# Kernel optimization log

Hardware: AMD Instinct MI355X
Metric: run time of the kernel (lower is better)

Reference implementation:

```python
import jax, jax.numpy as jnp
import numpy as np

D_MODEL = 512
NUM_HEADS = 8
D_K = D_MODEL // NUM_HEADS


def setup_inputs() -> dict:
    key = jax.random.key(0)
    kx, kq, kk, kv, ko = jax.random.split(key, 5)
    scale = 1.0 / np.sqrt(D_MODEL)
    return {
        "x": jax.random.normal(kx, (2, 4096, D_MODEL), dtype=jnp.float32),
        "Wq": jax.random.normal(kq, (D_MODEL, D_MODEL), dtype=jnp.float32) * scale,
        "Wk": jax.random.normal(kk, (D_MODEL, D_MODEL), dtype=jnp.float32) * scale,
        "Wv": jax.random.normal(kv, (D_MODEL, D_MODEL), dtype=jnp.float32) * scale,
        "Wo": jax.random.normal(ko, (D_MODEL, D_MODEL), dtype=jnp.float32) * scale,
    }


def reference(x, Wq, Wk, Wv, Wo):
    B, T, D = x.shape
    H, dk = NUM_HEADS, D_K
    # Linear(d,d, bias=False): y = x @ W.T ; weights stored [out,in] like torch
    q = (x @ Wq.T).reshape(B, T, H, dk).transpose(0, 2, 1, 3)  # [B,H,T,dk]
    k = (x @ Wk.T).reshape(B, T, H, dk).transpose(0, 2, 1, 3)
    v = (x @ Wv.T).reshape(B, T, H, dk).transpose(0, 2, 1, 3)
    scores = jnp.einsum("bhqd,bhkd->bhqk", q, k) / np.sqrt(dk)  # [B,H,T,T]
    probs = jax.nn.softmax(scores, axis=-1)
    o = jnp.einsum("bhqk,bhkd->bhqd", probs, v)  # [B,H,T,dk]
    o = o.transpose(0, 2, 1, 3).reshape(B, T, D)
    return o @ Wo.T
```

## Files before the change

### kernel.cpp

```cpp
#include <hip/hip_runtime.h>
#include <hip/hip_bf16.h>

#define SEQ 4096
#define DMODEL 512
#define HEADS 8
#define DK 64
#define BATCH 2
#define MTOT (BATCH * SEQ)
#define NBH (BATCH * HEADS)

typedef __attribute__((ext_vector_type(8))) short bh8;
typedef __attribute__((ext_vector_type(4))) float f4;
typedef __attribute__((ext_vector_type(16))) float f16x;

#define MFMA(a, b, c)   __builtin_amdgcn_mfma_f32_16x16x32_bf16(a, b, c, 0, 0, 0)
#define MFMA32(a, b, c) __builtin_amdgcn_mfma_f32_32x32x16_bf16(a, b, c, 0, 0, 0)
#define GLL16(g, l) __builtin_amdgcn_global_load_lds( \
    (const __attribute__((address_space(1))) void*)(g), \
    (__attribute__((address_space(3))) void*)(l), 16, 0, 0)

__device__ __forceinline__ unsigned short f2b(float f) {
    union { float f; unsigned u; } v; v.f = f;
    unsigned r = v.u + 0x7fff + ((v.u >> 16) & 1);
    return (unsigned short)(r >> 16);
}

__device__ __forceinline__ unsigned cvtpk(float lo, float hi) {
    unsigned r;
    asm("v_cvt_pk_bf16_f32 %0, %1, %2" : "=v"(r) : "v"(lo), "v"(hi));
    return r;
}
__device__ __forceinline__ void plswap(unsigned& a, unsigned& b) {
    asm("v_permlane32_swap_b32 %0, %1" : "+v"(a), "+v"(b));
}
__device__ __forceinline__ float wave_max_pair(float x) {
    float b = x; asm("" : "+v"(b));
    float a = x;
    asm("v_permlane32_swap_b32 %0, %1" : "+v"(a), "+v"(b));
    return fmaxf(a, b);
}
__device__ __forceinline__ float wave_sum_pair(float x) {
    float b = x; asm("" : "+v"(b));
    float a = x;
    asm("v_permlane32_swap_b32 %0, %1" : "+v"(a), "+v"(b));
    return a + b;
}

__global__ __launch_bounds__(256) void convert_k(
    const float* __restrict__ x, const float* __restrict__ wq,
    const float* __restrict__ wk, const float* __restrict__ wv,
    const float* __restrict__ wo, unsigned short* __restrict__ dst)
{
    const size_t i = ((size_t)blockIdx.x * 256 + threadIdx.x) * 4;
    const float* s; size_t o;
    if (i < 4194304u)                 { s = x;  o = i; }
    else if (i < 4194304u + 262144u)  { s = wq; o = i - 4194304u; }
    else if (i < 4194304u + 524288u)  { s = wk; o = i - (4194304u + 262144u); }
    else if (i < 4194304u + 786432u)  { s = wv; o = i - (4194304u + 524288u); }
    else                              { s = wo; o = i - (4194304u + 786432u); }
    float4 v = *(const float4*)(s + o);
    ushort4 u; u.x = f2b(v.x); u.y = f2b(v.y); u.z = f2b(v.z); u.w = f2b(v.w);
    *(ushort4*)(dst + i) = u;
}

__global__ __launch_bounds__(256) void qkv_gemm_mfma(
    const unsigned short* __restrict__ xb,
    const unsigned short* __restrict__ Wb,
    unsigned short* __restrict__ QKV)
{
    const int z = blockIdx.z;
    const unsigned short* A = xb;
    const unsigned short* B = Wb + (size_t)z * (DMODEL * DMODEL);
    const int m0 = blockIdx.x * 128, n0 = blockIdx.y * 128;
    const int tid = threadIdx.x, w = tid >> 6, l = tid & 63;
    const int wr = w >> 1, wc = w & 1;

    __shared__ __align__(16) unsigned short As[128 * 32];
    __shared__ __align__(16) unsigned short Bs[128 * 32];

    f4 acc[4][4] = {};
    const int lrow = l >> 2, lslot = l & 3;

    for (int k0 = 0; k0 < DMODEL; k0 += 32) {
        __syncthreads();
        #pragma unroll
        for (int j = 0; j < 2; ++j) {
            const int row = w * 32 + j * 16 + lrow;
            const int sw = lslot ^ ((row >> 1) & 3);
            GLL16(A + (size_t)(m0 + row) * DMODEL + k0 + sw * 8,
                  (char*)As + (w * 32 + j * 16) * 64);
            GLL16(B + (size_t)(n0 + row) * DMODEL + k0 + sw * 8,
                  (char*)Bs + (w * 32 + j * 16) * 64);
        }
        __syncthreads();
        bh8 af[4], bg[4];
        #pragma unroll
        for (int mi = 0; mi < 4; ++mi) {
            const int r = wr * 64 + mi * 16 + (l & 15);
            af[mi] = *(const bh8*)((const char*)As + r * 64 +
                                   (((l >> 4) * 16) ^ (((r >> 1) & 3) << 4)));
        }
        #pragma unroll
        for (int ni = 0; ni < 4; ++ni) {
            const int r = wc * 64 + ni * 16 + (l & 15);
            bg[ni] = *(const bh8*)((const char*)Bs + r * 64 +
                                   (((l >> 4) * 16) ^ (((r >> 1) & 3) << 4)));
        }
        #pragma unroll
        for (int mi = 0; mi < 4; ++mi)
            #pragma unroll
            for (int ni = 0; ni < 4; ++ni)
                acc[mi][ni] = MFMA(af[mi], bg[ni], acc[mi][ni]);
    }

    unsigned short* Out = QKV + (size_t)z * ((size_t)NBH * SEQ * DK);
    const float sc = (z == 0) ? 0.18033688011112042f : 1.0f;
    #pragma unroll
    for (int mi = 0; mi < 4; ++mi) {
        #pragma unroll
        for (int rg = 0; rg < 4; ++rg) {
            const int m = m0 + wr * 64 + mi * 16 + (l >> 4) * 4 + rg;
            const int b = m >> 12, t = m & (SEQ - 1);
            #pragma unroll
            for (int ni = 0; ni < 4; ++ni) {
                const int n = n0 + wc * 64 + ni * 16 + (l & 15);
                const int h = n >> 6, d = n & 63;
                Out[(((size_t)(b * HEADS + h)) * SEQ + t) * DK + d] =
                    f2b(acc[mi][ni][rg] * sc);
            }
        }
    }
}

__global__ __launch_bounds__(256) void vtrans(
    const unsigned short* __restrict__ Vh, unsigned short* __restrict__ Vt)
{
    const int bh = blockIdx.y, t0 = blockIdx.x * 64;
    __shared__ unsigned short L[64][72];
    const unsigned short* src = Vh + ((size_t)bh * SEQ + t0) * DK;
    const int r = threadIdx.x >> 3, c8 = (threadIdx.x & 7) * 8;
    #pragma unroll
    for (int it = 0; it < 2; ++it) {
        const int row = r + it * 32;
        ushort4 a = *(const ushort4*)(src + (size_t)row * DK + c8);
        ushort4 b = *(const ushort4*)(src + (size_t)row * DK + c8 + 4);
        L[row][c8 + 0] = a.x; L[row][c8 + 1] = a.y; L[row][c8 + 2] = a.z; L[row][c8 + 3] = a.w;
        L[row][c8 + 4] = b.x; L[row][c8 + 5] = b.y; L[row][c8 + 6] = b.z; L[row][c8 + 7] = b.w;
    }
    __syncthreads();
    unsigned short* dst = Vt + (size_t)bh * DK * SEQ + t0;
    #pragma unroll
    for (int it = 0; it < 2; ++it) {
        const int d = r + it * 32;
        ushort4 a, b;
        a.x = L[c8 + 0][d]; a.y = L[c8 + 1][d]; a.z = L[c8 + 2][d]; a.w = L[c8 + 3][d];
        b.x = L[c8 + 4][d]; b.y = L[c8 + 5][d]; b.z = L[c8 + 6][d]; b.w = L[c8 + 7][d];
        *(ushort4*)(dst + (size_t)d * SEQ + c8) = a;
        *(ushort4*)(dst + (size_t)d * SEQ + c8 + 4) = b;
    }
}

__global__ __launch_bounds__(256) void flash_mfma(
    const unsigned short* __restrict__ Qh,
    const unsigned short* __restrict__ Kh,
    const unsigned short* __restrict__ Vtp,
    unsigned short* __restrict__ Ow)
{
    const int bid = blockIdx.x;
    const int bh = bid & 15, q0 = (bid >> 4) * 128;
    const int tid = threadIdx.x, w = tid >> 6, l = tid & 63;
    const int lq = l & 31, hi = l >> 5;

    __shared__ __align__(16) unsigned short Ks[2][64 * 64];
    __shared__ __align__(16) unsigned short Vs[2][64 * 64];

    const unsigned short* Qb = Qh + (size_t)bh * SEQ * DK;
    const unsigned short* Kb = Kh + (size_t)bh * SEQ * DK;
    const unsigned short* Vb = Vtp + (size_t)bh * DK * SEQ;

    bh8 qf[4];
    #pragma unroll
    for (int ks = 0; ks < 4; ++ks)
        qf[ks] = *(const bh8*)(Qb + (size_t)(q0 + w * 32 + lq) * DK + ks * 16 + hi * 8);

    f16x o0 = {}, o1 = {};
    float m_run = -3.0e38f, l_run = 0.f;

    const int srow = l >> 3, sslot = l & 7;

#define STAGE(buf, kv0_) do {                                                 \
    _Pragma("unroll")                                                         \
    for (int j_ = 0; j_ < 2; ++j_) {                                          \
        const int row_ = w * 16 + j_ * 8 + srow;                              \
        const int sw_ = sslot ^ (row_ & 7);                                   \
        GLL16(Kb + (size_t)((kv0_) + row_) * DK + sw_ * 8,                    \
              (char*)Ks[buf] + (w * 16 + j_ * 8) * 128);                      \
        GLL16(Vb + (size_t)row_ * SEQ + (kv0_) + sw_ * 8,                     \
              (char*)Vs[buf] + (w * 16 + j_ * 8) * 128);                      \
    }                                                                         \
} while (0)

    STAGE(0, 0);
    __syncthreads();
    int cur = 0;

    for (int t = 0; t < SEQ / 64; ++t) {
        if (t < SEQ / 64 - 1) STAGE(cur ^ 1, (t + 1) * 64);

        const char* kb = (const char*)Ks[cur];
        const char* vb = (const char*)Vs[cur];

        f16x sa0 = {}, sa1 = {};
        __builtin_amdgcn_s_setprio(1);
        #pragma unroll
        for (int ks = 0; ks < 4; ++ks) {
            const int boff = ks * 32 + hi * 16;
            const int r0 = lq, r1 = 32 + lq;
            bh8 k0 = *(const bh8*)(kb + r0 * 128 + (boff ^ ((r0 & 7) << 4)));
            bh8 k1 = *(const bh8*)(kb + r1 * 128 + (boff ^ ((r1 & 7) << 4)));
            sa0 = MFMA32(k0, qf[ks], sa0);
            sa1 = MFMA32(k1, qf[ks], sa1);
        }
        __builtin_amdgcn_s_setprio(0);

        float t0 = -3.0e38f, t1 = -3.0e38f, t2 = -3.0e38f, t3 = -3.0e38f;
        #pragma unroll
        for (int r = 0; r < 16; r += 4) {
            t0 = fmaxf(t0, fmaxf(sa0[r + 0], sa1[r + 0]));
            t1 = fmaxf(t1, fmaxf(sa0[r + 1], sa1[r + 1]));
            t2 = fmaxf(t2, fmaxf(sa0[r + 2], sa1[r + 2]));
            t3 = fmaxf(t3, fmaxf(sa0[r + 3], sa1[r + 3]));
        }
        const float mx = wave_max_pair(fmaxf(fmaxf(t0, t1), fmaxf(t2, t3)));

        const bool skip = __all(mx <= m_run + 8.0f);
        float mnew = m_run, corr = 1.0f;
        if (!skip) {
            mnew = fmaxf(m_run, mx);
            corr = __builtin_amdgcn_exp2f(m_run - mnew);
        }

        float p[32];
        #pragma unroll
        for (int r = 0; r < 16; ++r) {
            p[r]      = __builtin_amdgcn_exp2f(sa0[r] - mnew);
            p[16 + r] = __builtin_amdgcn_exp2f(sa1[r] - mnew);
        }
        float a0 = 0.f, a1 = 0.f, a2 = 0.f, a3 = 0.f;
        #pragma unroll
        for (int r = 0; r < 32; r += 4) {
            a0 += p[r + 0]; a1 += p[r + 1]; a2 += p[r + 2]; a3 += p[r + 3];
        }
        const float psum = wave_sum_pair((a0 + a1) + (a2 + a3));

        if (!skip) {
            m_run = mnew;
            l_run = l_run * corr + psum;
            #pragma unroll
            for (int r = 0; r < 16; ++r) { o0[r] *= corr; o1[r] *= corr; }
        } else {
            l_run += psum;
        }

        bh8 pf[4];
        #pragma unroll
        for (int cb = 0; cb < 2; ++cb) {
            const int b0 = cb * 16;
            unsigned k0 = cvtpk(p[b0 + 0],  p[b0 + 1]);
            unsigned k1 = cvtpk(p[b0 + 2],  p[b0 + 3]);
            unsigned k2 = cvtpk(p[b0 + 4],  p[b0 + 5]);
            unsigned k3 = cvtpk(p[b0 + 6],  p[b0 + 7]);
            unsigned k4 = cvtpk(p[b0 + 8],  p[b0 + 9]);
            unsigned k5 = cvtpk(p[b0 + 10], p[b0 + 11]);
            unsigned k6 = cvtpk(p[b0 + 12], p[b0 + 13]);
            unsigned k7 = cvtpk(p[b0 + 14], p[b0 + 15]);
            plswap(k0, k2);
            plswap(k1, k3);
            plswap(k4, k6);
            plswap(k5, k7);
            union { unsigned u[4]; bh8 v; } f0, f1;
            f0.u[0] = k0; f0.u[1] = k1; f0.u[2] = k2; f0.u[3] = k3;
            f1.u[0] = k4; f1.u[1] = k5; f1.u[2] = k6; f1.u[3] = k7;
            pf[cb * 2 + 0] = f0.v;
            pf[cb * 2 + 1] = f1.v;
        }

        __builtin_amdgcn_s_setprio(1);
        #pragma unroll
        for (int ks = 0; ks < 4; ++ks) {
            const int boff = ks * 32 + hi * 16;
            const int r0 = lq, r1 = 32 + lq;
            bh8 v0 = *(const bh8*)(vb + r0 * 128 + (boff ^ ((r0 & 7) << 4)));
            bh8 v1 = *(const bh8*)(vb + r1 * 128 + (boff ^ ((r1 & 7) << 4)));
            o0 = MFMA32(v0, pf[ks], o0);
            o1 = MFMA32(v1, pf[ks], o1);
        }
        __builtin_amdgcn_s_setprio(0);

        __syncthreads();
        cur ^= 1;
    }
#undef STAGE

    const float inv = 1.0f / l_run;
    char* Tb = (char*)Ks + w * 4096;
    #pragma unroll
    for (int db = 0; db < 2; ++db) {
        f16x ov = db ? o1 : o0;
        #pragma unroll
        for (int j = 0; j < 8; ++j) {
            const int r = 2 * j;
            const int d = db * 32 + (r & 3) + 8 * (r >> 2) + 4 * hi;
            unsigned pk = cvtpk(ov[r] * inv, ov[r + 1] * inv);
            *(unsigned*)(Tb + lq * 128 + ((d * 2) ^ ((lq & 7) << 4))) = pk;
        }
    }
    __syncthreads();
    const int b = bh >> 3, h = bh & 7;
    const int row = l >> 1, half = l & 1;
    const int q = q0 + w * 32 + row;
    unsigned short* dst = Ow + ((size_t)b * SEQ + q) * DMODEL + h * DK + half * 32;
    #pragma unroll
    for (int i = 0; i < 4; ++i) {
        const int byte = (half * 64 + i * 16) ^ ((row & 7) << 4);
        uint4 vv = *(const uint4*)(Tb + row * 128 + byte);
        *(uint4*)(dst + i * 8) = vv;
    }
}

__global__ __launch_bounds__(256) void out_gemm_mfma(
    const unsigned short* __restrict__ Ob,
    const unsigned short* __restrict__ Wob,
    float* __restrict__ out)
{
    const int m0 = blockIdx.x * 128, n0 = blockIdx.y * 128;
    const int tid = threadIdx.x, w = tid >> 6, l = tid & 63;
    const int wr = w >> 1, wc = w & 1;

    __shared__ __align__(16) unsigned short As[128 * 32];
    __shared__ __align__(16) unsigned short Bs[128 * 32];

    f4 acc[4][4] = {};
    const int lrow = l >> 2, lslot = l & 3;

    for (int k0 = 0; k0 < DMODEL; k0 += 32) {
        __syncthreads();
        #pragma unroll
        for (int j = 0; j < 2; ++j) {
            const int row = w * 32 + j * 16 + lrow;
            const int sw = lslot ^ ((row >> 1) & 3);
            GLL16(Ob + (size_t)(m0 + row) * DMODEL + k0 + sw * 8,
                  (char*)As + (w * 32 + j * 16) * 64);
            GLL16(Wob + (size_t)(n0 + row) * DMODEL + k0 + sw * 8,
                  (char*)Bs + (w * 32 + j * 16) * 64);
        }
        __syncthreads();
        bh8 af[4], bg[4];
        #pragma unroll
        for (int mi = 0; mi < 4; ++mi) {
            const int r = wr * 64 + mi * 16 + (l & 15);
            af[mi] = *(const bh8*)((const char*)As + r * 64 +
                                   (((l >> 4) * 16) ^ (((r >> 1) & 3) << 4)));
        }
        #pragma unroll
        for (int ni = 0; ni < 4; ++ni) {
            const int r = wc * 64 + ni * 16 + (l & 15);
            bg[ni] = *(const bh8*)((const char*)Bs + r * 64 +
                                   (((l >> 4) * 16) ^ (((r >> 1) & 3) << 4)));
        }
        #pragma unroll
        for (int mi = 0; mi < 4; ++mi)
            #pragma unroll
            for (int ni = 0; ni < 4; ++ni)
                acc[mi][ni] = MFMA(af[mi], bg[ni], acc[mi][ni]);
    }

    #pragma unroll
    for (int mi = 0; mi < 4; ++mi) {
        #pragma unroll
        for (int rg = 0; rg < 4; ++rg) {
            const int m = m0 + wr * 64 + mi * 16 + (l >> 4) * 4 + rg;
            #pragma unroll
            for (int ni = 0; ni < 4; ++ni) {
                const int n = n0 + wc * 64 + ni * 16 + (l & 15);
                out[(size_t)m * DMODEL + n] = acc[mi][ni][rg];
            }
        }
    }
}

extern "C" void kernel_launch(void* const* d_in, const int* in_sizes, int n_in,
                              void* d_out, int out_size, void* d_ws, size_t ws_size,
                              hipStream_t stream)
{
    const float* x  = (const float*)d_in[0];
    const float* Wq = (const float*)d_in[1];
    const float* Wk = (const float*)d_in[2];
    const float* Wv = (const float*)d_in[3];
    const float* Wo = (const float*)d_in[4];
    float* out = (float*)d_out;

    unsigned short* ws = (unsigned short*)d_ws;
    unsigned short* xb  = ws;
    unsigned short* Wb  = xb + 4194304;
    unsigned short* QKV = Wb + 4 * 262144;
    unsigned short* Vt  = QKV + 3 * 4194304;
    unsigned short* Ow  = Vt + 4194304;
    unsigned short* Qh = QKV;
    unsigned short* Kh = QKV + 4194304;
    unsigned short* Vh = QKV + 2 * 4194304;

    convert_k<<<5120, 256, 0, stream>>>(x, Wq, Wk, Wv, Wo, ws);
    qkv_gemm_mfma<<<dim3(MTOT / 128, DMODEL / 128, 3), 256, 0, stream>>>(xb, Wb, QKV);
    vtrans<<<dim3(SEQ / 64, NBH), 256, 0, stream>>>(Vh, Vt);
    flash_mfma<<<512, 256, 0, stream>>>(Qh, Kh, Vt, Ow);
    out_gemm_mfma<<<dim3(MTOT / 128, DMODEL / 128), 256, 0, stream>>>(
        Ow, Wb + 3 * 262144, out);
}
```

Measured before the change: 145.4 us.

## Stage K/V tiles in MFMA-fragment order and pack softmax math

The K and V tiles are now loaded into LDS already arranged as per-lane MFMA fragments, so each lane reads contiguous 16-byte chunks at fixed offsets. This replaces the swizzled row addressing and its XOR math, and the global loads become less contiguous per row. The softmax inner loop also uses v_max3 for the row max and packed f32 add and multiply for the subtract, the sum and the output rescale. These cut VALU instruction count in the loop between the MFMAs.

Measured after the change: 154.0 us. 1.06x slower.

```diff
diff --git a/kernel.cpp b/kernel.cpp
--- a/kernel.cpp
+++ b/kernel.cpp
@@ -12,6 +12,7 @@
 typedef __attribute__((ext_vector_type(8))) short bh8;
 typedef __attribute__((ext_vector_type(4))) float f4;
 typedef __attribute__((ext_vector_type(16))) float f16x;
+typedef __attribute__((ext_vector_type(2))) float f2;
 
 #define MFMA(a, b, c)   __builtin_amdgcn_mfma_f32_16x16x32_bf16(a, b, c, 0, 0, 0)
 #define MFMA32(a, b, c) __builtin_amdgcn_mfma_f32_32x32x16_bf16(a, b, c, 0, 0, 0)
@@ -44,6 +45,16 @@
     float a = x;
     asm("v_permlane32_swap_b32 %0, %1" : "+v"(a), "+v"(b));
     return a + b;
+}
+__device__ __forceinline__ f2 pk_add(f2 a, f2 b) {
+    f2 d; asm("v_pk_add_f32 %0, %1, %2" : "=v"(d) : "v"(a), "v"(b)); return d;
+}
+__device__ __forceinline__ f2 pk_mul(f2 a, f2 b) {
+    f2 d; asm("v_pk_mul_f32 %0, %1, %2" : "=v"(d) : "v"(a), "v"(b)); return d;
+}
+__device__ __forceinline__ float max3f(float a, float b, float c) {
+    float d; asm("v_max3_f32 %0, %1, %2, %3" : "=v"(d) : "v"(a), "v"(b), "v"(c));
+    return d;
 }
 
 __global__ __launch_bounds__(256) void convert_k(
@@ -171,8 +182,7 @@
     const int tid = threadIdx.x, w = tid >> 6, l = tid & 63;
     const int lq = l & 31, hi = l >> 5;
 
-    __shared__ __align__(16) unsigned short Ks[2][64 * 64];
-    __shared__ __align__(16) unsigned short Vs[2][64 * 64];
+    __shared__ __align__(16) char lds[32768];
 
     const unsigned short* Qb = Qh + (size_t)bh * SEQ * DK;
     const unsigned short* Kb = Kh + (size_t)bh * SEQ * DK;
@@ -183,55 +193,56 @@
     for (int ks = 0; ks < 4; ++ks)
         qf[ks] = *(const bh8*)(Qb + (size_t)(q0 + w * 32 + lq) * DK + ks * 16 + hi * 8);
 
+    int koff[2], voff[2];
+    #pragma unroll
+    for (int j = 0; j < 2; ++j) {
+        const int f = 2 * w + j, rh = f >> 2, ks = f & 3;
+        koff[j] = (rh * 32 + lq) * DK + ks * 16 + hi * 8;
+        voff[j] = (rh * 32 + lq) * SEQ + ks * 16 + hi * 8;
+    }
+
     f16x o0 = {}, o1 = {};
     float m_run = -3.0e38f, l_run = 0.f;
 
-    const int srow = l >> 3, sslot = l & 7;
-
-#define STAGE(buf, kv0_) do {                                                 \
-    _Pragma("unroll")                                                         \
-    for (int j_ = 0; j_ < 2; ++j_) {                                          \
-        const int row_ = w * 16 + j_ * 8 + srow;                              \
-        const int sw_ = sslot ^ (row_ & 7);                                   \
-        GLL16(Kb + (size_t)((kv0_) + row_) * DK + sw_ * 8,                    \
-              (char*)Ks[buf] + (w * 16 + j_ * 8) * 128);                      \
-        GLL16(Vb + (size_t)row_ * SEQ + (kv0_) + sw_ * 8,                     \
-              (char*)Vs[buf] + (w * 16 + j_ * 8) * 128);                      \
-    }                                                                         \
+#define STAGE(buf, kv0_) do {                                             \
+    _Pragma("unroll")                                                     \
+    for (int j_ = 0; j_ < 2; ++j_) {                                      \
+        GLL16(Kb + (size_t)(kv0_) * DK + koff[j_],                        \
+              lds + (buf) * 16384 + (2 * w + j_) * 1024);                 \
+        GLL16(Vb + (size_t)(kv0_) + voff[j_],                             \
+              lds + (buf) * 16384 + 8192 + (2 * w + j_) * 1024);          \
+    }                                                                     \
 } while (0)
 
     STAGE(0, 0);
     __syncthreads();
     int cur = 0;
+    const char* myfrag = lds + l * 16;
 
     for (int t = 0; t < SEQ / 64; ++t) {
         if (t < SEQ / 64 - 1) STAGE(cur ^ 1, (t + 1) * 64);
 
-        const char* kb = (const char*)Ks[cur];
-        const char* vb = (const char*)Vs[cur];
+        const char* kb = myfrag + cur * 16384;
 
         f16x sa0 = {}, sa1 = {};
         __builtin_amdgcn_s_setprio(1);
         #pragma unroll
         for (int ks = 0; ks < 4; ++ks) {
-            const int boff = ks * 32 + hi * 16;
-            const int r0 = lq, r1 = 32 + lq;
-            bh8 k0 = *(const bh8*)(kb + r0 * 128 + (boff ^ ((r0 & 7) << 4)));
-            bh8 k1 = *(const bh8*)(kb + r1 * 128 + (boff ^ ((r1 & 7) << 4)));
+            bh8 k0 = *(const bh8*)(kb + ks * 1024);
+            bh8 k1 = *(const bh8*)(kb + (4 + ks) * 1024);
             sa0 = MFMA32(k0, qf[ks], sa0);
             sa1 = MFMA32(k1, qf[ks], sa1);
         }
         __builtin_amdgcn_s_setprio(0);
 
-        float t0 = -3.0e38f, t1 = -3.0e38f, t2 = -3.0e38f, t3 = -3.0e38f;
-        #pragma unroll
-        for (int r = 0; r < 16; r += 4) {
-            t0 = fmaxf(t0, fmaxf(sa0[r + 0], sa1[r + 0]));
-            t1 = fmaxf(t1, fmaxf(sa0[r + 1], sa1[r + 1]));
-            t2 = fmaxf(t2, fmaxf(sa0[r + 2], sa1[r + 2]));
-            t3 = fmaxf(t3, fmaxf(sa0[r + 3], sa1[r + 3]));
-        }
-        const float mx = wave_max_pair(fmaxf(fmaxf(t0, t1), fmaxf(t2, t3)));
+        float a = fmaxf(sa0[0], sa0[1]);
+        float b = fmaxf(sa1[0], sa1[1]);
+        #pragma unroll
+        for (int r = 2; r < 16; r += 2) {
+            a = max3f(a, sa0[r], sa0[r + 1]);
+            b = max3f(b, sa1[r], sa1[r + 1]);
+        }
+        const float mx = wave_max_pair(fmaxf(a, b));
 
         const bool skip = __all(mx <= m_run + 8.0f);
         float mnew = m_run, corr = 1.0f;
@@ -240,24 +251,43 @@
             corr = __builtin_amdgcn_exp2f(m_run - mnew);
         }
 
-        float p[32];
-        #pragma unroll
-        for (int r = 0; r < 16; ++r) {
-            p[r]      = __builtin_amdgcn_exp2f(sa0[r] - mnew);
-            p[16 + r] = __builtin_amdgcn_exp2f(sa1[r] - mnew);
-        }
-        float a0 = 0.f, a1 = 0.f, a2 = 0.f, a3 = 0.f;
-        #pragma unroll
-        for (int r = 0; r < 32; r += 4) {
-            a0 += p[r + 0]; a1 += p[r + 1]; a2 += p[r + 2]; a3 += p[r + 3];
-        }
-        const float psum = wave_sum_pair((a0 + a1) + (a2 + a3));
+        union uf { f16x v; f2 h[8]; };
+        uf U0, U1; U0.v = sa0; U1.v = sa1;
+        f2 nm2; nm2[0] = -mnew; nm2[1] = -mnew;
+        f2 p2[16];
+        #pragma unroll
+        for (int i = 0; i < 8; ++i) {
+            f2 t0 = pk_add(U0.h[i], nm2);
+            f2 t1 = pk_add(U1.h[i], nm2);
+            f2 e0, e1;
+            e0[0] = __builtin_amdgcn_exp2f(t0[0]);
+            e0[1] = __builtin_amdgcn_exp2f(t0[1]);
+            e1[0] = __builtin_amdgcn_exp2f(t1[0]);
+            e1[1] = __builtin_amdgcn_exp2f(t1[1]);
+            p2[i] = e0; p2[8 + i] = e1;
+        }
+
+        f2 s0 = pk_add(p2[0], p2[1]),   s1 = pk_add(p2[2], p2[3]);
+        f2 s2 = pk_add(p2[4], p2[5]),   s3 = pk_add(p2[6], p2[7]);
+        f2 s4 = pk_add(p2[8], p2[9]),   s5 = pk_add(p2[10], p2[11]);
+        f2 s6 = pk_add(p2[12], p2[13]), s7 = pk_add(p2[14], p2[15]);
+        s0 = pk_add(s0, s1); s2 = pk_add(s2, s3);
+        s4 = pk_add(s4, s5); s6 = pk_add(s6, s7);
+        s0 = pk_add(s0, s2); s4 = pk_add(s4, s6);
+        s0 = pk_add(s0, s4);
+        const float psum = wave_sum_pair(s0[0] + s0[1]);
 
         if (!skip) {
             m_run = mnew;
             l_run = l_run * corr + psum;
+            f2 c2; c2[0] = corr; c2[1] = corr;
+            uf O0, O1; O0.v = o0; O1.v = o1;
             #pragma unroll
-            for (int r = 0; r < 16; ++r) { o0[r] *= corr; o1[r] *= corr; }
+            for (int i = 0; i < 8; ++i) {
+                O0.h[i] = pk_mul(O0.h[i], c2);
+                O1.h[i] = pk_mul(O1.h[i], c2);
+            }
+            o0 = O0.v; o1 = O1.v;
         } else {
             l_run += psum;
         }
@@ -265,19 +295,15 @@
         bh8 pf[4];
         #pragma unroll
         for (int cb = 0; cb < 2; ++cb) {
-            const int b0 = cb * 16;
-            unsigned k0 = cvtpk(p[b0 + 0],  p[b0 + 1]);
-            unsigned k1 = cvtpk(p[b0 + 2],  p[b0 + 3]);
-            unsigned k2 = cvtpk(p[b0 + 4],  p[b0 + 5]);
-            unsigned k3 = cvtpk(p[b0 + 6],  p[b0 + 7]);
-            unsigned k4 = cvtpk(p[b0 + 8],  p[b0 + 9]);
-            unsigned k5 = cvtpk(p[b0 + 10], p[b0 + 11]);
-            unsigned k6 = cvtpk(p[b0 + 12], p[b0 + 13]);
-            unsigned k7 = cvtpk(p[b0 + 14], p[b0 + 15]);
-            plswap(k0, k2);
-            plswap(k1, k3);
-            plswap(k4, k6);
-            plswap(k5, k7);
+            unsigned k0 = cvtpk(p2[8 * cb + 0][0], p2[8 * cb + 0][1]);
+            unsigned k1 = cvtpk(p2[8 * cb + 1][0], p2[8 * cb + 1][1]);
+            unsigned k2 = cvtpk(p2[8 * cb + 2][0], p2[8 * cb + 2][1]);
+            unsigned k3 = cvtpk(p2[8 * cb + 3][0], p2[8 * cb + 3][1]);
+            unsigned k4 = cvtpk(p2[8 * cb + 4][0], p2[8 * cb + 4][1]);
+            unsigned k5 = cvtpk(p2[8 * cb + 5][0], p2[8 * cb + 5][1]);
+            unsigned k6 = cvtpk(p2[8 * cb + 6][0], p2[8 * cb + 6][1]);
+            unsigned k7 = cvtpk(p2[8 * cb + 7][0], p2[8 * cb + 7][1]);
+            plswap(k0, k2); plswap(k1, k3); plswap(k4, k6); plswap(k5, k7);
             union { unsigned u[4]; bh8 v; } f0, f1;
             f0.u[0] = k0; f0.u[1] = k1; f0.u[2] = k2; f0.u[3] = k3;
             f1.u[0] = k4; f1.u[1] = k5; f1.u[2] = k6; f1.u[3] = k7;
@@ -285,13 +311,12 @@
             pf[cb * 2 + 1] = f1.v;
         }
 
+        const char* vb = myfrag + cur * 16384 + 8192;
         __builtin_amdgcn_s_setprio(1);
         #pragma unroll
         for (int ks = 0; ks < 4; ++ks) {
-            const int boff = ks * 32 + hi * 16;
-            const int r0 = lq, r1 = 32 + lq;
-            bh8 v0 = *(const bh8*)(vb + r0 * 128 + (boff ^ ((r0 & 7) << 4)));
-            bh8 v1 = *(const bh8*)(vb + r1 * 128 + (boff ^ ((r1 & 7) << 4)));
+            bh8 v0 = *(const bh8*)(vb + ks * 1024);
+            bh8 v1 = *(const bh8*)(vb + (4 + ks) * 1024);
             o0 = MFMA32(v0, pf[ks], o0);
             o1 = MFMA32(v1, pf[ks], o1);
         }
@@ -303,7 +328,7 @@
 #undef STAGE
 
     const float inv = 1.0f / l_run;
-    char* Tb = (char*)Ks + w * 4096;
+    char* Tb = lds + w * 4096;
     #pragma unroll
     for (int db = 0; db < 2; ++db) {
         f16x ov = db ? o1 : o0;
```
